# Kernel optimization log

Measured on AMD Instinct MI355X. Metric: run time of the kernel, lower is better.

The kernel has to match this reference:

```python
import jax, jax.numpy as jnp
import numpy as np


def setup_inputs() -> dict:
    key = jax.random.key(0)
    k1, k2, k3, k4 = jax.random.split(key, 4)
    B, T, I, H = 64, 512, 256, 512
    stdv = 1.0 / np.sqrt(H)
    x = jax.random.normal(k1, (B, T, I), dtype=jnp.float32)
    weight_ih = jax.random.uniform(k2, (I, 4 * H), dtype=jnp.float32, minval=-stdv, maxval=stdv)
    weight_hh = jax.random.uniform(k3, (H, 4 * H), dtype=jnp.float32, minval=-stdv, maxval=stdv)
    bias_ih = jax.random.uniform(k4, (4 * H,), dtype=jnp.float32, minval=-stdv, maxval=stdv)
    return {"x": x, "weight_ih": weight_ih, "weight_hh": weight_hh, "bias_ih": bias_ih}


def reference(x, weight_ih, weight_hh, bias_ih):
    B, T, I = x.shape
    H = weight_hh.shape[0]
    # Precompute input projections for all timesteps: [T, B, 4H]
    x_proj = jnp.einsum('bti,ig->tbg', x, weight_ih) + bias_ih

    def step(carry, xp):
        h, c = carry
        gates = xp + h @ weight_hh  # [B, 4H]
        ig, fg, cg, og = jnp.split(gates, 4, axis=1)
        ig = jax.nn.sigmoid(ig)
        fg = jax.nn.sigmoid(fg)
        cg = jnp.tanh(cg)
        # NOTE: original code applies NO sigmoid to outgate and adds it:
        # hy = outgate * tanh(cy) + outgate
        cy = fg * c + ig * cg
        hy = og * jnp.tanh(cy) + og
        return (hy, cy), hy

    h0 = jnp.zeros((B, H), dtype=x.dtype)
    c0 = jnp.zeros((B, H), dtype=x.dtype)
    _, hs = jax.lax.scan(step, (h0, c0), x_proj)  # hs: [T, B, H]
    return jnp.transpose(hs, (1, 0, 2))  # [B, T, H]
```

## Files before the change

### kernel.cpp

```cpp
#include <hip/hip_runtime.h>
#include <hip/hip_bf16.h>
#include <math.h>

#define BB 64
#define TT 512
#define II 256
#define HH 512
#define GG 2048
#define NBLK 128
#define KP  520
#define XPAD 264

typedef unsigned char u8;
typedef unsigned short u16;
typedef unsigned long long u64;
typedef __attribute__((ext_vector_type(4))) int   i32x4;
typedef __attribute__((ext_vector_type(4))) short short4v;
typedef __attribute__((ext_vector_type(8))) short short8v;
typedef __attribute__((ext_vector_type(4))) float f32x4;

__device__ __forceinline__ u16 f2bf(float f) {
    unsigned u = __float_as_uint(f);
    unsigned r = (u + 0x7fff + ((u >> 16) & 1)) >> 16;
    return (u16)r;
}
__device__ __forceinline__ float bf2f(u16 h) {
    return __uint_as_float(((unsigned)h) << 16);
}
__device__ __forceinline__ float sigf(float v) {
    return 1.f / (1.f + __expf(-v));
}
__device__ __forceinline__ float tanh_s(float v) {
    float a = fabsf(v);
    float e = __expf(2.f * a);
    float r = 1.f - 2.f / (e + 1.f);
    return copysignf(r, v);
}

#define HLD(dst, base, OFF) \
    asm volatile("global_load_dwordx4 %0, %1, off offset:" OFF " sc0 sc1" \
                 : "=v"(dst) : "v"(base))

__global__ void __launch_bounds__(64, 1) slstm_kernel(
    const float* __restrict__ x, const float* __restrict__ wih,
    const float* __restrict__ whh, const float* __restrict__ bias,
    float* __restrict__ out, u8* __restrict__ flagb,
    u16* __restrict__ hbuf )
{
    __shared__ u16 lds_whh[4 * 16 * KP];
    __shared__ u16 lds_wih[64 * XPAD];
    __shared__ u16 lds_x[16 * XPAD];

    const int l  = threadIdx.x;
    const int bt = blockIdx.x & 3;
    const int js = blockIdx.x >> 2;
    const int b0 = bt * 16, j0 = js * 16;
    const int c  = l & 15, kq = l >> 4;

    for (int q = 0; q < 4; ++q)
        for (int kk = 0; kk < 128; ++kk) {
            int k = kk * 4 + kq;
            lds_whh[(q * 16 + c) * KP + k] =
                f2bf(whh[(size_t)k * GG + q * 512 + j0 + c]);
        }
    for (int q = 0; q < 4; ++q)
        for (int kk = 0; kk < 64; ++kk) {
            int k = kk * 4 + kq;
            lds_wih[(q * 16 + c) * XPAD + k] =
                f2bf(wih[(size_t)k * GG + q * 512 + j0 + c]);
        }

    float bq[4];
#pragma unroll
    for (int q = 0; q < 4; ++q) bq[q] = bias[q * 512 + j0 + c];

    float cst[4] = {0.f, 0.f, 0.f, 0.f};
    __syncthreads();

    for (int t = 0; t < TT; ++t) {
#pragma unroll 4
        for (int r = 0; r < 16; ++r) {
            float4 v = *(const float4*)(x + ((size_t)(b0 + r) * TT + t) * II + 4 * l);
            short4v p;
            p[0] = (short)f2bf(v.x); p[1] = (short)f2bf(v.y);
            p[2] = (short)f2bf(v.z); p[3] = (short)f2bf(v.w);
            *(short4v*)&lds_x[r * XPAD + 4 * l] = p;
        }
        __syncthreads();

        f32x4 acc[4];
#pragma unroll
        for (int q = 0; q < 4; ++q) acc[q] = (f32x4){bq[q], bq[q], bq[q], bq[q]};
#pragma unroll
        for (int s = 0; s < 8; ++s) {
            short8v a = *(const short8v*)&lds_x[c * XPAD + 32 * s + 8 * kq];
#pragma unroll
            for (int q = 0; q < 4; ++q) {
                short8v b = *(const short8v*)&lds_wih[(q * 16 + c) * XPAD + 32 * s + 8 * kq];
                acc[q] = __builtin_amdgcn_mfma_f32_16x16x32_bf16(a, b, acc[q], 0, 0, 0);
            }
        }

        if (t > 0) {
            const u8* fb = flagb + ((size_t)(bt * TT + (t - 1))) * 32;
            while (true) {
                i32x4 w0, w1;
                asm volatile(
                    "global_load_dwordx4 %0, %2, off sc0 sc1\n\t"
                    "global_load_dwordx4 %1, %2, off offset:16 sc0 sc1\n\t"
                    "s_waitcnt vmcnt(0)"
                    : "=v"(w0), "=v"(w1) : "v"(fb) : "memory");
                int m = w0[0] & w0[1] & w0[2] & w0[3] & w1[0] & w1[1] & w1[2] & w1[3];
                if (m == 0x01010101) break;
                __builtin_amdgcn_s_sleep(1);
            }
        }
        __builtin_amdgcn_sched_barrier(0);

        const int rp = (t - 1) & 1;
        const u16* hb = hbuf + (size_t)(rp * 2) * BB * HH + (size_t)(b0 + c) * HH + 8 * kq;
        const u16* lb = hb + BB * HH;
        i32x4 h0,h1,h2,h3,h4,h5,h6,h7,h8,h9,h10,h11,h12,h13,h14,h15;
        i32x4 g0,g1,g2,g3,g4,g5,g6,g7,g8,g9,g10,g11,g12,g13,g14,g15;
        HLD(h0, hb,   "0"); HLD(g0, lb,   "0");
        HLD(h1, hb,  "64"); HLD(g1, lb,  "64");
        HLD(h2, hb, "128"); HLD(g2, lb, "128");
        HLD(h3, hb, "192"); HLD(g3, lb, "192");
        HLD(h4, hb, "256"); HLD(g4, lb, "256");
        HLD(h5, hb, "320"); HLD(g5, lb, "320");
        HLD(h6, hb, "384"); HLD(g6, lb, "384");
        HLD(h7, hb, "448"); HLD(g7, lb, "448");
        HLD(h8, hb, "512"); HLD(g8, lb, "512");
        HLD(h9, hb, "576"); HLD(g9, lb, "576");
        HLD(h10,hb, "640"); HLD(g10,lb, "640");
        HLD(h11,hb, "704"); HLD(g11,lb, "704");
        HLD(h12,hb, "768"); HLD(g12,lb, "768");
        HLD(h13,hb, "832"); HLD(g13,lb, "832");
        HLD(h14,hb, "896"); HLD(g14,lb, "896");
        HLD(h15,hb, "960"); HLD(g15,lb, "960");

#define HMM(S, FH, FL) do {                                                     \
        short8v ah_ = __builtin_bit_cast(short8v, FH);                          \
        short8v al_ = __builtin_bit_cast(short8v, FL);                          \
        _Pragma("unroll")                                                       \
        for (int q = 0; q < 4; ++q) {                                           \
            short8v b_ = *(const short8v*)&lds_whh[(q * 16 + c) * KP + 32 * (S) + 8 * kq]; \
            acc[q] = __builtin_amdgcn_mfma_f32_16x16x32_bf16(ah_, b_, acc[q], 0, 0, 0); \
            acc[q] = __builtin_amdgcn_mfma_f32_16x16x32_bf16(al_, b_, acc[q], 0, 0, 0); \
        }                                                                       \
    } while (0)

        asm volatile("s_waitcnt vmcnt(16)" ::: "memory");
        __builtin_amdgcn_sched_barrier(0);
        HMM(0, h0, g0); HMM(1, h1, g1); HMM(2, h2, g2); HMM(3, h3, g3);
        HMM(4, h4, g4); HMM(5, h5, g5); HMM(6, h6, g6); HMM(7, h7, g7);
        asm volatile("s_waitcnt vmcnt(0)" ::: "memory");
        __builtin_amdgcn_sched_barrier(0);
        HMM(8, h8, g8); HMM(9, h9, g9); HMM(10,h10,g10); HMM(11,h11,g11);
        HMM(12,h12,g12); HMM(13,h13,g13); HMM(14,h14,g14); HMM(15,h15,g15);

        const int wp = t & 1;
        u16* hdst_hi = hbuf + (size_t)(wp * 2) * BB * HH;
        u16* hdst_lo = hdst_hi + BB * HH;
        const int j = j0 + c;
#pragma unroll
        for (int rg = 0; rg < 4; ++rg) {
            int b = b0 + kq * 4 + rg;
            float ig = sigf(acc[0][rg]);
            float fg = sigf(acc[1][rg]);
            float cg = tanh_s(acc[2][rg]);
            float og = acc[3][rg];
            float cy = fg * cst[rg] + ig * cg;
            cst[rg] = cy;
            float hy = og * tanh_s(cy) + og;
            out[((size_t)b * TT + t) * HH + j] = hy;
            u16 hi = f2bf(hy);
            float lo = hy - bf2f(hi);
            __hip_atomic_store(&hdst_hi[(size_t)b * HH + j], hi,
                               __ATOMIC_RELAXED, __HIP_MEMORY_SCOPE_AGENT);
            __hip_atomic_store(&hdst_lo[(size_t)b * HH + j], f2bf(lo),
                               __ATOMIC_RELAXED, __HIP_MEMORY_SCOPE_AGENT);
        }
        asm volatile("s_waitcnt vmcnt(0)" ::: "memory");
        if (l == 0)
            __hip_atomic_store(flagb + ((size_t)(bt * TT + t)) * 32 + js, (u8)1,
                               __ATOMIC_RELAXED, __HIP_MEMORY_SCOPE_AGENT);
    }
}

extern "C" void kernel_launch(void* const* d_in, const int* in_sizes, int n_in,
                              void* d_out, int out_size, void* d_ws, size_t ws_size,
                              hipStream_t stream) {
    const float* x    = (const float*)d_in[0];
    const float* wih  = (const float*)d_in[1];
    const float* whh  = (const float*)d_in[2];
    const float* bias = (const float*)d_in[3];
    float* out = (float*)d_out;

    u8*  flagb = (u8*)d_ws;
    u16* hbuf  = (u16*)((char*)d_ws + 65536);
    size_t clear = 65536 + (size_t)2 * 2 * BB * HH * sizeof(u16);
    hipMemsetAsync(d_ws, 0, clear, stream);

    hipLaunchKernelGGL(slstm_kernel, dim3(NBLK), dim3(64), 0, stream,
                       x, wih, whh, bias, out, flagb, hbuf);
}
```

Measured before the change: 2.865 ms.

## Prefetch next timestep's x into registers and issue flag poll early

Loads x for timestep t+1 into registers while step t runs, then converts it to bf16 with v_cvt_pk_bf16_f32 and writes it to LDS at the end of the step. This takes the x load latency off the critical path of the recurrence. The first flag-poll load is also issued before the input-projection MFMAs, so its latency overlaps that compute. The per-step __syncthreads is dropped, which is safe only because the kernel runs a single wave of 64 threads. The change also relies on vmcnt ordering across the inline-asm loads and raises register pressure.

```diff
diff --git a/kernel.cpp b/kernel.cpp
--- a/kernel.cpp
+++ b/kernel.cpp
@@ -13,8 +13,10 @@
 
 typedef unsigned char u8;
 typedef unsigned short u16;
+typedef unsigned int u32;
 typedef unsigned long long u64;
 typedef __attribute__((ext_vector_type(4))) int   i32x4;
+typedef __attribute__((ext_vector_type(2))) int   i32x2;
 typedef __attribute__((ext_vector_type(4))) short short4v;
 typedef __attribute__((ext_vector_type(8))) short short8v;
 typedef __attribute__((ext_vector_type(4))) float f32x4;
@@ -40,6 +42,11 @@
 #define HLD(dst, base, OFF) \
     asm volatile("global_load_dwordx4 %0, %1, off offset:" OFF " sc0 sc1" \
                  : "=v"(dst) : "v"(base))
+#define XLD(dst, voff, sbase) \
+    asm volatile("global_load_dwordx4 %0, %1, %2" \
+                 : "=v"(dst) : "v"(voff), "s"(sbase))
+#define CVTPK(d, lo, hi) \
+    asm("v_cvt_pk_bf16_f32 %0, %1, %2" : "=v"(d) : "v"(lo), "v"(hi))
 
 __global__ void __launch_bounds__(64, 1) slstm_kernel(
     const float* __restrict__ x, const float* __restrict__ wih,
@@ -77,16 +84,41 @@
     float cst[4] = {0.f, 0.f, 0.f, 0.f};
     __syncthreads();
 
+    const u32 vbase = (u32)(b0 * TT * II * 4) + 16 * (u32)l;
+
+    f32x4 xr[16];
+#pragma unroll
+    for (int r = 0; r < 16; ++r) {
+        u32 vo = vbase + (u32)(r * TT * II * 4);
+        XLD(xr[r], vo, x);
+    }
+    asm volatile("s_waitcnt vmcnt(0)" ::: "memory");
+    __builtin_amdgcn_sched_barrier(0);
+#pragma unroll
+    for (int r = 0; r < 16; ++r) {
+        i32x2 p;
+        CVTPK(p[0], xr[r][0], xr[r][1]);
+        CVTPK(p[1], xr[r][2], xr[r][3]);
+        *(i32x2*)&lds_x[r * XPAD + 4 * l] = p;
+    }
+
     for (int t = 0; t < TT; ++t) {
-#pragma unroll 4
+        i32x4 w0, w1;
+        const u8* fb = flagb;
+        if (t > 0) {
+            fb = flagb + ((size_t)(bt * TT + (t - 1))) * 32;
+            asm volatile(
+                "global_load_dwordx4 %0, %2, off sc0 sc1\n\t"
+                "global_load_dwordx4 %1, %2, off offset:16 sc0 sc1"
+                : "=v"(w0), "=v"(w1) : "v"(fb) : "memory");
+        }
+
+        const int tn = (t + 1 < TT) ? t + 1 : TT - 1;
+#pragma unroll
         for (int r = 0; r < 16; ++r) {
-            float4 v = *(const float4*)(x + ((size_t)(b0 + r) * TT + t) * II + 4 * l);
-            short4v p;
-            p[0] = (short)f2bf(v.x); p[1] = (short)f2bf(v.y);
-            p[2] = (short)f2bf(v.z); p[3] = (short)f2bf(v.w);
-            *(short4v*)&lds_x[r * XPAD + 4 * l] = p;
-        }
-        __syncthreads();
+            u32 vo = vbase + (u32)(r * TT * II * 4) + (u32)(tn * II * 4);
+            XLD(xr[r], vo, x);
+        }
 
         f32x4 acc[4];
 #pragma unroll
@@ -102,20 +134,20 @@
         }
 
         if (t > 0) {
-            const u8* fb = flagb + ((size_t)(bt * TT + (t - 1))) * 32;
-            while (true) {
-                i32x4 w0, w1;
+            asm volatile("s_waitcnt vmcnt(16)" ::: "memory");
+            __builtin_amdgcn_sched_barrier(0);
+            int m = w0[0] & w0[1] & w0[2] & w0[3] & w1[0] & w1[1] & w1[2] & w1[3];
+            while (m != 0x01010101) {
+                __builtin_amdgcn_s_sleep(1);
                 asm volatile(
                     "global_load_dwordx4 %0, %2, off sc0 sc1\n\t"
                     "global_load_dwordx4 %1, %2, off offset:16 sc0 sc1\n\t"
                     "s_waitcnt vmcnt(0)"
                     : "=v"(w0), "=v"(w1) : "v"(fb) : "memory");
-                int m = w0[0] & w0[1] & w0[2] & w0[3] & w1[0] & w1[1] & w1[2] & w1[3];
-                if (m == 0x01010101) break;
-                __builtin_amdgcn_s_sleep(1);
+                m = w0[0] & w0[1] & w0[2] & w0[3] & w1[0] & w1[1] & w1[2] & w1[3];
             }
-        }
-        __builtin_amdgcn_sched_barrier(0);
+            __builtin_amdgcn_sched_barrier(0);
+        }
 
         const int rp = (t - 1) & 1;
         const u16* hb = hbuf + (size_t)(rp * 2) * BB * HH + (size_t)(b0 + c) * HH + 8 * kq;
@@ -181,6 +213,15 @@
             __hip_atomic_store(&hdst_lo[(size_t)b * HH + j], f2bf(lo),
                                __ATOMIC_RELAXED, __HIP_MEMORY_SCOPE_AGENT);
         }
+
+#pragma unroll
+        for (int r = 0; r < 16; ++r) {
+            i32x2 p;
+            CVTPK(p[0], xr[r][0], xr[r][1]);
+            CVTPK(p[1], xr[r][2], xr[r][3]);
+            *(i32x2*)&lds_x[r * XPAD + 4 * l] = p;
+        }
+
         asm volatile("s_waitcnt vmcnt(0)" ::: "memory");
         if (l == 0)
             __hip_atomic_store(flagb + ((size_t)(bt * TT + t)) * 32 + js, (u8)1,
```

New measurement: 2.549 ms. 1.12x faster.
